# Performance work log

Hardware: AMD Instinct MI355X
Metric: run time of the kernel (lower is better)

Reference implementation:

```python
import jax, jax.numpy as jnp
import numpy as np

NUM_CLASSES = [5, 7, 4, 6, 3, 8, 5, 4, 6, 7, 3, 5, 4, 6, 8, 5, 7, 4, 6, 3]
N_ONE_HOTS = 20
N_OTHERS = 30
H = 48
W = 48
B = 128
N_MAP = 32
ENC_OUT = 32
RES_C = 128
OH_EMB = 9
SUM_NC = sum(NUM_CLASSES)  # 106


def conv2d(x, w, b=None, pad=0):
    # x: NCHW, w: OIHW
    y = jax.lax.conv_general_dilated(
        x, w, window_strides=(1, 1), padding=[(pad, pad), (pad, pad)],
        dimension_numbers=('NCHW', 'OIHW', 'NCHW'))
    if b is not None:
        y = y + b[None, :, None, None]
    return y


def setup_inputs() -> dict:
    key = jax.random.key(0)
    ks = jax.random.split(key, 20)
    x = jax.random.normal(ks[0], (B, 1 + N_MAP, H, W), dtype=jnp.float32)
    # first N_ONE_HOTS entries of flattened channel 0 are categorical indices
    idx_cols = [jax.random.randint(jax.random.fold_in(ks[1], j), (B,), 0, nc)
                for j, nc in enumerate(NUM_CLASSES)]
    idx = jnp.stack(idx_cols, axis=1).astype(jnp.float32)  # (B, 20)
    x = x.at[:, 0, 0, :N_ONE_HOTS].set(idx)
    s = 0.05
    inp = {
        'x': x,
        'fc_w': jax.random.normal(ks[2], (OH_EMB, SUM_NC), jnp.float32) * s,
        'fc_b': jnp.zeros((OH_EMB,), jnp.float32),
        'oh_conv_w': jax.random.normal(ks[3], (OH_EMB, OH_EMB, 1, 1), jnp.float32) * s,
        'oh_conv_b': jnp.zeros((OH_EMB,), jnp.float32),
        'others_conv_w': jax.random.normal(ks[4], (N_OTHERS, N_OTHERS, 1, 1), jnp.float32) * s,
        'others_conv_b': jnp.zeros((N_OTHERS,), jnp.float32),
        'all_conv_w': jax.random.normal(ks[5], (ENC_OUT, OH_EMB + N_OTHERS, 1, 1), jnp.float32) * s,
        'all_conv_b': jnp.zeros((ENC_OUT,), jnp.float32),
        'conv1_w': jax.random.normal(ks[6], (RES_C, ENC_OUT + N_MAP, 1, 1), jnp.float32) * s,
        'conv1_b': jnp.zeros((RES_C,), jnp.float32),
        'rconv1_w': jax.random.normal(ks[7], (RES_C, RES_C, 5, 5), jnp.float32) * s,
        'rconv1_b': jnp.zeros((RES_C,), jnp.float32),
        'rconv2_w': jax.random.normal(ks[8], (RES_C, RES_C, 5, 5), jnp.float32) * s,
        'rconv2_b': jnp.zeros((RES_C,), jnp.float32),
        'se_w1': jax.random.normal(ks[9], (RES_C // 16, RES_C), jnp.float32) * s,
        'se_w2': jax.random.normal(ks[10], (RES_C, RES_C // 16), jnp.float32) * s,
    }
    return inp


def reference(x, fc_w, fc_b, oh_conv_w, oh_conv_b, others_conv_w, others_conv_b,
              all_conv_w, all_conv_b, conv1_w, conv1_b, rconv1_w, rconv1_b,
              rconv2_w, rconv2_b, se_w1, se_w2):
    b = x.shape[0]
    gi = x[:, 0].reshape(b, -1)                 # (b, H*W)
    map_feature = x[:, 1:]                      # (b, N_MAP, H, W)
    idx = jax.lax.stop_gradient(gi[:, :N_ONE_HOTS]).astype(jnp.int32)
    others = gi[:, N_ONE_HOTS:N_ONE_HOTS + N_OTHERS]   # (b, 30)
    # vectorized one-hot build (replaces the quadratic python loop)
    oh = jnp.concatenate(
        [jax.nn.one_hot(idx[:, j], nc, dtype=x.dtype) for j, nc in enumerate(NUM_CLASSES)],
        axis=1)                                 # (b, SUM_NC)
    v = oh @ fc_w.T + fc_b                      # (b, 9)
    # faithful torch expand((h,w)+shape).reshape((b,-1,h,w)) semantics
    v = jnp.broadcast_to(v, (H, W, b, OH_EMB)).reshape(b, OH_EMB, H, W)
    o = jnp.broadcast_to(others, (H, W, b, N_OTHERS)).reshape(b, N_OTHERS, H, W)
    v = conv2d(v, oh_conv_w, oh_conv_b)
    o = conv2d(o, others_conv_w, others_conv_b)
    gi_map = conv2d(jnp.concatenate([v, o], axis=1), all_conv_w, all_conv_b)  # (b, 32, H, W)
    h = conv2d(jnp.concatenate([gi_map, map_feature], axis=1), conv1_w, conv1_b)  # (b, 128, H, W)
    # residual block: 5x5 convs, LeakyReLU, SE, identity skip (in==out)
    identity = h
    y = jax.nn.leaky_relu(conv2d(h, rconv1_w, rconv1_b, pad=2))
    y = conv2d(y, rconv2_w, rconv2_b, pad=2)
    s = y.mean(axis=(2, 3))                     # (b, 128)
    s = jax.nn.sigmoid(jax.nn.relu(s @ se_w1.T) @ se_w2.T)
    y = y * s[:, :, None, None]
    return jax.nn.leaky_relu(y + identity)
```

## Files before the change

### kernel.cpp

```cpp
#include <hip/hip_runtime.h>
#include <hip/hip_bf16.h>
#include <cstddef>

#define HH 48
#define WW 48
#define PIX 2304
#define BB 128
#define RESC 128
#define XCH 33

typedef short bf16x8 __attribute__((ext_vector_type(8)));
typedef float f32x4 __attribute__((ext_vector_type(4)));

static __device__ __forceinline__ float b2f(unsigned short u) {
    unsigned x = ((unsigned)u) << 16;
    return __builtin_bit_cast(float, x);
}
static __device__ __forceinline__ unsigned short f2b(float f) {
    __hip_bfloat16 hb = __float2bfloat16(f);
    return __builtin_bit_cast(unsigned short, hb);
}

__global__ void k_compute_v(const float* __restrict__ x, const float* __restrict__ fc_w,
                            const float* __restrict__ fc_b, float* __restrict__ v) {
    int b = blockIdx.x * blockDim.x + threadIdx.x;
    if (b >= BB) return;
    const int off[20] = {0,5,12,16,22,25,33,38,42,48,55,58,63,67,73,81,86,93,97,103};
    const float* gi = x + (size_t)b * XCH * PIX;
    int cols[20];
    #pragma unroll
    for (int j = 0; j < 20; j++) cols[j] = off[j] + (int)gi[j];
    #pragma unroll
    for (int e = 0; e < 9; e++) {
        float acc = fc_b[e];
        #pragma unroll
        for (int j = 0; j < 20; j++) acc += fc_w[e * 106 + cols[j]];
        v[b * 9 + e] = acc;
    }
}

__global__ void k_compute_G(const float* __restrict__ x, const float* __restrict__ v,
                            const float* __restrict__ ohw, const float* __restrict__ ohb,
                            const float* __restrict__ otw, const float* __restrict__ otb,
                            const float* __restrict__ aw,  const float* __restrict__ ab,
                            const float* __restrict__ c1w, const float* __restrict__ c1b,
                            float* __restrict__ G) {
    int p = blockIdx.x * blockDim.x + threadIdx.x;
    if (p >= PIX) return;
    float sv = v[((p / 9) & 127) * 9 + (p % 9)];
    float om[30];
    #pragma unroll
    for (int c2 = 0; c2 < 30; c2++) {
        int tmp = c2 * 24 + p;
        int c = tmp % 30;
        int bb = (c2 * 76 + tmp / 30) & 127;
        om[c2] = x[(size_t)bb * XCH * PIX + 20 + c];
    }
    float v9[9];
    #pragma unroll
    for (int e = 0; e < 9; e++) {
        float srow = 0.f;
        #pragma unroll
        for (int e2 = 0; e2 < 9; e2++) srow += ohw[e * 9 + e2];
        v9[e] = ohb[e] + srow * sv;
    }
    float o30[30];
    #pragma unroll
    for (int c = 0; c < 30; c++) {
        float a = otb[c];
        #pragma unroll
        for (int c2 = 0; c2 < 30; c2++) a += otw[c * 30 + c2] * om[c2];
        o30[c] = a;
    }
    float gi32[32];
    #pragma unroll
    for (int g = 0; g < 32; g++) {
        float a = ab[g];
        #pragma unroll
        for (int e = 0; e < 9; e++) a += aw[g * 39 + e] * v9[e];
        #pragma unroll
        for (int c = 0; c < 30; c++) a += aw[g * 39 + 9 + c] * o30[c];
        gi32[g] = a;
    }
    for (int oc = 0; oc < 128; oc++) {
        float a = c1b[oc];
        #pragma unroll
        for (int g = 0; g < 32; g++) a += c1w[oc * 64 + g] * gi32[g];
        G[p * 128 + oc] = a;
    }
}

__global__ void k_convert_w(const float* __restrict__ w1, const float* __restrict__ w2,
                            __hip_bfloat16* __restrict__ wb1, __hip_bfloat16* __restrict__ wb2) {
    int i = blockIdx.x * 256 + threadIdx.x;
    if (i >= 25 * 128 * 128) return;
    int tap = i / 16384, r = i % 16384;
    int oc = r >> 7, ic = r & 127;
    size_t src = (size_t)(oc * 128 + ic) * 25 + tap;
    wb1[i] = __float2bfloat16(w1[src]);
    wb2[i] = __float2bfloat16(w2[src]);
}

__global__ __launch_bounds__(256) void k_conv1(const float* __restrict__ x, const float* __restrict__ c1w,
                                               const float* __restrict__ G, __hip_bfloat16* __restrict__ h) {
    __shared__ float xm[32][64];
    __shared__ float w1[32][128];
    int b = blockIdx.y, p0 = blockIdx.x * 64;
    int t = threadIdx.x;
    for (int i = t; i < 4096; i += 256) { int m = i >> 7, oc = i & 127; w1[m][oc] = c1w[oc * 64 + 32 + m]; }
    for (int i = t; i < 2048; i += 256) {
        int m = i >> 6, pix = i & 63;
        xm[m][pix] = x[(size_t)b * XCH * PIX + (size_t)(1 + m) * PIX + p0 + pix];
    }
    __syncthreads();
    int pix = t & 63, ocg = t >> 6;
    float acc[32] = {};
    for (int m = 0; m < 32; m++) {
        float xv = xm[m][pix];
        const float4* wr = (const float4*)&w1[m][ocg * 32];
        #pragma unroll
        for (int k4 = 0; k4 < 8; k4++) {
            float4 wv = wr[k4];
            acc[k4 * 4 + 0] += wv.x * xv; acc[k4 * 4 + 1] += wv.y * xv;
            acc[k4 * 4 + 2] += wv.z * xv; acc[k4 * 4 + 3] += wv.w * xv;
        }
    }
    size_t hb = ((size_t)b * PIX + p0 + pix) * 128 + ocg * 32;
    const float* gp = &G[(size_t)(p0 + pix) * 128 + ocg * 32];
    #pragma unroll
    for (int q = 0; q < 4; q++) {
        unsigned short u[8];
        #pragma unroll
        for (int j = 0; j < 8; j++) u[j] = f2b(acc[q * 8 + j] + gp[q * 8 + j]);
        *(uint4*)(&h[hb + q * 8]) = *(uint4*)u;
    }
}

template<bool LEAKY, bool MEAN>
__global__ __launch_bounds__(256, 2) void k_conv5_mfma(
        const __hip_bfloat16* __restrict__ in,
        const __hip_bfloat16* __restrict__ w,
        const float* __restrict__ bias,
        __hip_bfloat16* __restrict__ out,
        float* __restrict__ mean) {
    __shared__ __align__(16) char lds[20 * 20 * 64 * 2];
    int b = blockIdx.z, tile = blockIdx.x;
    int ty0 = (tile / 3) * 16, tx0 = (tile % 3) * 16;
    int t = threadIdx.x;
    int wave = t >> 6, lane = t & 63;
    int wm = wave & 1, wn = wave >> 1;
    int l15 = lane & 15, lg = lane >> 4;

    f32x4 acc[4][8] = {};
    const size_t inb = (size_t)b * PIX * 128;

    for (int icb = 0; icb < 128; icb += 64) {
        if (icb) __syncthreads();
        for (int i = t; i < 3200; i += 256) {
            int s = i >> 3, c16 = i & 7;
            int ry = s / 20, rx = s % 20;
            int gy = ty0 - 2 + ry, gx = tx0 - 2 + rx;
            uint4 val = {0, 0, 0, 0};
            if ((unsigned)gy < 48u && (unsigned)gx < 48u)
                val = *(const uint4*)(in + inb + (size_t)(gy * 48 + gx) * 128 + icb + c16 * 8);
            int byte = ((s << 7) + (c16 << 4)) ^ ((s & 7) << 4);
            *(uint4*)(lds + byte) = val;
        }
        __syncthreads();
        for (int tap = 0; tap < 25; ++tap) {
            int dy = tap / 5, dx = tap % 5;
            const __hip_bfloat16* wt = w + (size_t)tap * 16384 + (size_t)(wm * 64 + l15) * 128 + icb + lg * 8;
            #pragma unroll
            for (int kk = 0; kk < 64; kk += 32) {
                bf16x8 A[4];
                #pragma unroll
                for (int m = 0; m < 4; m++) {
                    uint4 av = *(const uint4*)(wt + m * 16 * 128 + kk);
                    A[m] = __builtin_bit_cast(bf16x8, av);
                }
                #pragma unroll
                for (int n = 0; n < 8; n++) {
                    int s = (wn * 8 + n + dy) * 20 + (l15 + dx);
                    int byte = ((s << 7) + ((kk + lg * 8) << 1)) ^ ((s & 7) << 4);
                    bf16x8 B = *(const bf16x8*)(lds + byte);
                    #pragma unroll
                    for (int m = 0; m < 4; m++)
                        acc[m][n] = __builtin_amdgcn_mfma_f32_16x16x32_bf16(A[m], B, acc[m][n], 0, 0, 0);
                }
            }
        }
    }

    #pragma unroll
    for (int m = 0; m < 4; m++) {
        int ocm = wm * 64 + m * 16 + lg * 4;
        float b0 = bias[ocm], b1 = bias[ocm + 1], b2 = bias[ocm + 2], b3 = bias[ocm + 3];
        float ps0 = 0, ps1 = 0, ps2 = 0, ps3 = 0;
        #pragma unroll
        for (int n = 0; n < 8; n++) {
            float v0 = acc[m][n][0] + b0, v1 = acc[m][n][1] + b1;
            float v2 = acc[m][n][2] + b2, v3 = acc[m][n][3] + b3;
            ps0 += v0; ps1 += v1; ps2 += v2; ps3 += v3;
            if (LEAKY) {
                v0 = v0 > 0.f ? v0 : 0.01f * v0; v1 = v1 > 0.f ? v1 : 0.01f * v1;
                v2 = v2 > 0.f ? v2 : 0.01f * v2; v3 = v3 > 0.f ? v3 : 0.01f * v3;
            }
            int gp = (ty0 + wn * 8 + n) * 48 + tx0 + l15;
            uint2 pk;
            pk.x = (unsigned)f2b(v0) | ((unsigned)f2b(v1) << 16);
            pk.y = (unsigned)f2b(v2) | ((unsigned)f2b(v3) << 16);
            *(uint2*)(out + inb + (size_t)gp * 128 + ocm) = pk;
        }
        if (MEAN) {
            #pragma unroll
            for (int mask = 1; mask < 16; mask <<= 1) {
                ps0 += __shfl_xor(ps0, mask);
                ps1 += __shfl_xor(ps1, mask);
                ps2 += __shfl_xor(ps2, mask);
                ps3 += __shfl_xor(ps3, mask);
            }
            if (l15 == 0) {
                atomicAdd(&mean[b * 128 + ocm], ps0);
                atomicAdd(&mean[b * 128 + ocm + 1], ps1);
                atomicAdd(&mean[b * 128 + ocm + 2], ps2);
                atomicAdd(&mean[b * 128 + ocm + 3], ps3);
            }
        }
    }
}

__global__ void k_se(const float* __restrict__ mean, const float* __restrict__ w1,
                     const float* __restrict__ w2, float* __restrict__ s) {
    __shared__ float m[128];
    __shared__ float tt[8];
    int b = blockIdx.x, t = threadIdx.x;
    m[t] = mean[b * RESC + t] * (1.0f / 2304.0f);
    __syncthreads();
    if (t < 8) {
        float a = 0.f;
        for (int i = 0; i < 128; i++) a += w1[t * 128 + i] * m[i];
        tt[t] = a > 0.f ? a : 0.f;
    }
    __syncthreads();
    float a = 0.f;
    #pragma unroll
    for (int r = 0; r < 8; r++) a += w2[t * 8 + r] * tt[r];
    s[b * RESC + t] = 1.f / (1.f + expf(-a));
}

__global__ __launch_bounds__(256) void k_final(const __hip_bfloat16* __restrict__ y2,
                                               const __hip_bfloat16* __restrict__ h,
                                               const float* __restrict__ sg, float* __restrict__ out) {
    __shared__ float sl[128];
    __shared__ float tile[64 * 129];
    int b = blockIdx.y, p0 = blockIdx.x * 64, t = threadIdx.x;
    if (t < 128) sl[t] = sg[b * 128 + t];
    __syncthreads();
    const size_t base = ((size_t)b * PIX + p0) * 128;
    #pragma unroll
    for (int k = 0; k < 4; ++k) {
        int j = t + k * 256;
        int pix = j >> 4, c = j & 15;
        uint4 yv = *(const uint4*)(y2 + base + (size_t)pix * 128 + c * 8);
        uint4 hv = *(const uint4*)(h + base + (size_t)pix * 128 + c * 8);
        const unsigned short* yp = (const unsigned short*)&yv;
        const unsigned short* hp = (const unsigned short*)&hv;
        #pragma unroll
        for (int jj = 0; jj < 8; ++jj) {
            int oc = c * 8 + jj;
            tile[pix * 129 + oc] = b2f(yp[jj]) * sl[oc] + b2f(hp[jj]);
        }
    }
    __syncthreads();
    int oc = t >> 1, xh = (t & 1) * 32;
    float ov[32];
    #pragma unroll
    for (int i = 0; i < 32; ++i) {
        float v = tile[(xh + i) * 129 + oc];
        ov[i] = v > 0.f ? v : 0.01f * v;
    }
    float* op = out + ((size_t)b * 128 + oc) * PIX + p0 + xh;
    #pragma unroll
    for (int q = 0; q < 8; ++q) ((float4*)op)[q] = *(float4*)&ov[q * 4];
}

extern "C" void kernel_launch(void* const* d_in, const int* in_sizes, int n_in,
                              void* d_out, int out_size, void* d_ws, size_t ws_size,
                              hipStream_t stream) {
    const float* x      = (const float*)d_in[0];
    const float* fc_w   = (const float*)d_in[1];
    const float* fc_b   = (const float*)d_in[2];
    const float* ohw    = (const float*)d_in[3];
    const float* ohb    = (const float*)d_in[4];
    const float* otw    = (const float*)d_in[5];
    const float* otb    = (const float*)d_in[6];
    const float* aw     = (const float*)d_in[7];
    const float* ab     = (const float*)d_in[8];
    const float* c1w    = (const float*)d_in[9];
    const float* c1b    = (const float*)d_in[10];
    const float* r1w    = (const float*)d_in[11];
    const float* r1b    = (const float*)d_in[12];
    const float* r2w    = (const float*)d_in[13];
    const float* r2b    = (const float*)d_in[14];
    const float* se_w1  = (const float*)d_in[15];
    const float* se_w2  = (const float*)d_in[16];

    const size_t planeb = (size_t)BB * PIX * 128 * sizeof(__hip_bfloat16);
    char* ws = (char*)d_ws;
    __hip_bfloat16* h   = (__hip_bfloat16*)ws;  ws += planeb;
    __hip_bfloat16* y1  = (__hip_bfloat16*)ws;  ws += planeb;
    __hip_bfloat16* y2  = (__hip_bfloat16*)ws;  ws += planeb;
    float* G    = (float*)ws;                   ws += (size_t)PIX * 128 * sizeof(float);
    float* v    = (float*)ws;                   ws += (size_t)BB * 9 * sizeof(float);
    __hip_bfloat16* wb1 = (__hip_bfloat16*)ws;  ws += (size_t)25 * 128 * 128 * sizeof(__hip_bfloat16);
    __hip_bfloat16* wb2 = (__hip_bfloat16*)ws;  ws += (size_t)25 * 128 * 128 * sizeof(__hip_bfloat16);
    float* mean = (float*)ws;                   ws += (size_t)BB * RESC * sizeof(float);
    float* sgate= (float*)ws;                   ws += (size_t)BB * RESC * sizeof(float);

    k_compute_v<<<1, 128, 0, stream>>>(x, fc_w, fc_b, v);
    k_compute_G<<<9, 256, 0, stream>>>(x, v, ohw, ohb, otw, otb, aw, ab, c1w, c1b, G);
    k_convert_w<<<1600, 256, 0, stream>>>(r1w, r2w, wb1, wb2);
    k_conv1<<<dim3(36, 128), 256, 0, stream>>>(x, c1w, G, h);
    k_conv5_mfma<true, false><<<dim3(9, 1, 128), 256, 0, stream>>>(h, wb1, r1b, y1, nullptr);
    hipMemsetAsync(mean, 0, (size_t)BB * RESC * sizeof(float), stream);
    k_conv5_mfma<false, true><<<dim3(9, 1, 128), 256, 0, stream>>>(y1, wb2, r2b, y2, mean);
    k_se<<<128, 128, 0, stream>>>(mean, se_w1, se_w2, sgate);
    k_final<<<dim3(36, 128), 256, 0, stream>>>(y2, h, sgate, (float*)d_out);
}
```

Baseline: 834.4 us.

## Pad activations, double-buffer conv5 LDS via direct global-to-LDS loads

Stores h and y1 in a zero-bordered 52x52 padded layout so the 5x5 conv halo loads need no bounds checks. Each conv5 block now stages its input through global_load_lds into two 32-channel LDS buffers, so the next channel chunk loads while MFMAs run on the current one. Weight fragments for the next tap are prefetched into registers ahead of use, and s_setprio is raised around the MFMA bursts. In exchange it adds a border-zeroing kernel, slightly larger buffers and more complex swizzled address arithmetic.

```diff
diff --git a/kernel.cpp b/kernel.cpp
--- a/kernel.cpp
+++ b/kernel.cpp
@@ -5,6 +5,7 @@
 #define HH 48
 #define WW 48
 #define PIX 2304
+#define PPIX 2704
 #define BB 128
 #define RESC 128
 #define XCH 33
@@ -20,6 +21,10 @@
     __hip_bfloat16 hb = __float2bfloat16(f);
     return __builtin_bit_cast(unsigned short, hb);
 }
+
+#define GLOAD_LDS16(gp, lp) __builtin_amdgcn_global_load_lds( \
+    (const __attribute__((address_space(1))) void*)(gp), \
+    (__attribute__((address_space(3))) void*)(lp), 16, 0, 0)
 
 __global__ void k_compute_v(const float* __restrict__ x, const float* __restrict__ fc_w,
                             const float* __restrict__ fc_b, float* __restrict__ v) {
@@ -101,6 +106,20 @@
     wb2[i] = __float2bfloat16(w2[src]);
 }
 
+__global__ void k_zero_border(__hip_bfloat16* __restrict__ a, __hip_bfloat16* __restrict__ b2) {
+    int img = blockIdx.x, t = threadIdx.x;
+    for (int j = t; j < 6400; j += 256) {
+        int pb = j >> 4, c16 = j & 15;
+        int y, x2;
+        if (pb < 208) { int q = pb / 52; y = q < 2 ? q : q + 48; x2 = pb % 52; }
+        else { int r = pb - 208; y = 2 + (r >> 2); int c = r & 3; x2 = c < 2 ? c : c + 48; }
+        size_t off = ((size_t)img * PPIX + y * 52 + x2) * 128 + c16 * 8;
+        uint4 z = {0, 0, 0, 0};
+        *(uint4*)(a + off) = z;
+        *(uint4*)(b2 + off) = z;
+    }
+}
+
 __global__ __launch_bounds__(256) void k_conv1(const float* __restrict__ x, const float* __restrict__ c1w,
                                                const float* __restrict__ G, __hip_bfloat16* __restrict__ h) {
     __shared__ float xm[32][64];
@@ -125,8 +144,10 @@
             acc[k4 * 4 + 2] += wv.z * xv; acc[k4 * 4 + 3] += wv.w * xv;
         }
     }
-    size_t hb = ((size_t)b * PIX + p0 + pix) * 128 + ocg * 32;
-    const float* gp = &G[(size_t)(p0 + pix) * 128 + ocg * 32];
+    int p = p0 + pix;
+    int py = p / 48, px2 = p % 48;
+    size_t hb = ((size_t)b * PPIX + (py + 2) * 52 + px2 + 2) * 128 + ocg * 32;
+    const float* gp = &G[(size_t)p * 128 + ocg * 32];
     #pragma unroll
     for (int q = 0; q < 4; q++) {
         unsigned short u[8];
@@ -136,68 +157,112 @@
     }
 }
 
-template<bool LEAKY, bool MEAN>
+template<bool LEAKY, bool MEAN, bool PADOUT>
 __global__ __launch_bounds__(256, 2) void k_conv5_mfma(
         const __hip_bfloat16* __restrict__ in,
         const __hip_bfloat16* __restrict__ w,
         const float* __restrict__ bias,
         __hip_bfloat16* __restrict__ out,
         float* __restrict__ mean) {
-    __shared__ __align__(16) char lds[20 * 20 * 64 * 2];
+    __shared__ __align__(16) char lds[2][25600];
     int b = blockIdx.z, tile = blockIdx.x;
     int ty0 = (tile / 3) * 16, tx0 = (tile % 3) * 16;
-    int t = threadIdx.x;
-    int wave = t >> 6, lane = t & 63;
+    int t = threadIdx.x, lane = t & 63, wave = t >> 6;
     int wm = wave & 1, wn = wave >> 1;
     int l15 = lane & 15, lg = lane >> 4;
 
+    const size_t inb = (size_t)b * PPIX * 128;
+    const __hip_bfloat16* wbase = w + (size_t)(wm * 64 + l15) * 128 + lg * 8;
+
+    int sbase[8];
+    #pragma unroll
+    for (int n = 0; n < 8; ++n) sbase[n] = (wn * 8 + n) * 20 + l15;
+
     f32x4 acc[4][8] = {};
-    const size_t inb = (size_t)b * PIX * 128;
-
-    for (int icb = 0; icb < 128; icb += 64) {
-        if (icb) __syncthreads();
-        for (int i = t; i < 3200; i += 256) {
-            int s = i >> 3, c16 = i & 7;
+
+    auto stage = [&](int buf, int icb2) {
+        #pragma unroll
+        for (int k = 0; k < 6; ++k) {
+            int sg = k * 256 + t;
+            int u = sg >> 3, j = sg & 7;
+            int bb = j ^ (u & 7);
+            int s = (u << 1) | (bb >> 2);
+            int lg2 = bb & 3;
             int ry = s / 20, rx = s % 20;
-            int gy = ty0 - 2 + ry, gx = tx0 - 2 + rx;
-            uint4 val = {0, 0, 0, 0};
-            if ((unsigned)gy < 48u && (unsigned)gx < 48u)
-                val = *(const uint4*)(in + inb + (size_t)(gy * 48 + gx) * 128 + icb + c16 * 8);
-            int byte = ((s << 7) + (c16 << 4)) ^ ((s & 7) << 4);
-            *(uint4*)(lds + byte) = val;
-        }
-        __syncthreads();
-        for (int tap = 0; tap < 25; ++tap) {
-            int dy = tap / 5, dx = tap % 5;
-            const __hip_bfloat16* wt = w + (size_t)tap * 16384 + (size_t)(wm * 64 + l15) * 128 + icb + lg * 8;
-            #pragma unroll
-            for (int kk = 0; kk < 64; kk += 32) {
-                bf16x8 A[4];
-                #pragma unroll
-                for (int m = 0; m < 4; m++) {
-                    uint4 av = *(const uint4*)(wt + m * 16 * 128 + kk);
-                    A[m] = __builtin_bit_cast(bf16x8, av);
-                }
-                #pragma unroll
-                for (int n = 0; n < 8; n++) {
-                    int s = (wn * 8 + n + dy) * 20 + (l15 + dx);
-                    int byte = ((s << 7) + ((kk + lg * 8) << 1)) ^ ((s & 7) << 4);
-                    bf16x8 B = *(const bf16x8*)(lds + byte);
-                    #pragma unroll
-                    for (int m = 0; m < 4; m++)
-                        acc[m][n] = __builtin_amdgcn_mfma_f32_16x16x32_bf16(A[m], B, acc[m][n], 0, 0, 0);
-                }
-            }
-        }
-    }
-
-    #pragma unroll
-    for (int m = 0; m < 4; m++) {
+            const __hip_bfloat16* gp = in + inb + (size_t)((ty0 + ry) * 52 + tx0 + rx) * 128 + icb2 + lg2 * 8;
+            char* lp = &lds[buf][(k * 256 + (wave << 6)) * 16];
+            GLOAD_LDS16(gp, lp);
+        }
+        if (wave == 0) {
+            int sg = 1536 + lane;
+            int u = sg >> 3, j = sg & 7;
+            int bb = j ^ (u & 7);
+            int s = (u << 1) | (bb >> 2);
+            int lg2 = bb & 3;
+            int ry = s / 20, rx = s % 20;
+            const __hip_bfloat16* gp = in + inb + (size_t)((ty0 + ry) * 52 + tx0 + rx) * 128 + icb2 + lg2 * 8;
+            char* lp = &lds[buf][1536 * 16];
+            GLOAD_LDS16(gp, lp);
+        }
+    };
+
+#define AISSUE(Areg, tap_) do { \
+        const __hip_bfloat16* wp = wbase + (size_t)(tap_) * 16384 + icb; \
+        Areg[0] = *(const bf16x8*)(wp); \
+        Areg[1] = *(const bf16x8*)(wp + 2048); \
+        Areg[2] = *(const bf16x8*)(wp + 4096); \
+        Areg[3] = *(const bf16x8*)(wp + 6144); \
+    } while (0)
+
+#define CTAP(Areg, tap_) do { \
+        int toff = (tap_) + 15 * ((tap_) / 5); \
+        __builtin_amdgcn_s_setprio(1); \
+        _Pragma("unroll") \
+        for (int n = 0; n < 8; ++n) { \
+            int s = sbase[n] + toff; \
+            int u = s >> 1; \
+            int jj = (((s & 1) << 2) | lg) ^ (u & 7); \
+            bf16x8 Bv = *(const bf16x8*)(cb + (u << 7) + (jj << 4)); \
+            acc[0][n] = __builtin_amdgcn_mfma_f32_16x16x32_bf16(Areg[0], Bv, acc[0][n], 0, 0, 0); \
+            acc[1][n] = __builtin_amdgcn_mfma_f32_16x16x32_bf16(Areg[1], Bv, acc[1][n], 0, 0, 0); \
+            acc[2][n] = __builtin_amdgcn_mfma_f32_16x16x32_bf16(Areg[2], Bv, acc[2][n], 0, 0, 0); \
+            acc[3][n] = __builtin_amdgcn_mfma_f32_16x16x32_bf16(Areg[3], Bv, acc[3][n], 0, 0, 0); \
+        } \
+        __builtin_amdgcn_s_setprio(0); \
+    } while (0)
+
+    stage(0, 0);
+    __syncthreads();
+
+    for (int c = 0; c < 4; ++c) {
+        const int icb = c * 32;
+        const char* cb = lds[c & 1];
+        bf16x8 A0[4], A1[4];
+        AISSUE(A0, 0);
+        AISSUE(A1, 1);
+        __builtin_amdgcn_sched_barrier(0);
+        if (c < 3) stage((c + 1) & 1, icb + 32);
+        __builtin_amdgcn_sched_barrier(0);
+        for (int i = 0; i < 12; ++i) {
+            int tp = 2 * i;
+            CTAP(A0, tp);
+            AISSUE(A0, tp + 2);
+            CTAP(A1, tp + 1);
+            AISSUE(A1, tp + 3);
+        }
+        CTAP(A0, 24);
+        if (c < 3) __syncthreads();
+    }
+#undef AISSUE
+#undef CTAP
+
+    #pragma unroll
+    for (int m = 0; m < 4; ++m) {
         int ocm = wm * 64 + m * 16 + lg * 4;
         float b0 = bias[ocm], b1 = bias[ocm + 1], b2 = bias[ocm + 2], b3 = bias[ocm + 3];
         float ps0 = 0, ps1 = 0, ps2 = 0, ps3 = 0;
         #pragma unroll
-        for (int n = 0; n < 8; n++) {
+        for (int n = 0; n < 8; ++n) {
             float v0 = acc[m][n][0] + b0, v1 = acc[m][n][1] + b1;
             float v2 = acc[m][n][2] + b2, v3 = acc[m][n][3] + b3;
             ps0 += v0; ps1 += v1; ps2 += v2; ps3 += v3;
@@ -205,11 +270,14 @@
                 v0 = v0 > 0.f ? v0 : 0.01f * v0; v1 = v1 > 0.f ? v1 : 0.01f * v1;
                 v2 = v2 > 0.f ? v2 : 0.01f * v2; v3 = v3 > 0.f ? v3 : 0.01f * v3;
             }
-            int gp = (ty0 + wn * 8 + n) * 48 + tx0 + l15;
+            int row = ty0 + wn * 8 + n, col = tx0 + l15;
+            size_t off;
+            if (PADOUT) off = ((size_t)b * PPIX + (row + 2) * 52 + col + 2) * 128 + ocm;
+            else        off = ((size_t)b * PIX + row * 48 + col) * 128 + ocm;
             uint2 pk;
             pk.x = (unsigned)f2b(v0) | ((unsigned)f2b(v1) << 16);
             pk.y = (unsigned)f2b(v2) | ((unsigned)f2b(v3) << 16);
-            *(uint2*)(out + inb + (size_t)gp * 128 + ocm) = pk;
+            *(uint2*)(out + off) = pk;
         }
         if (MEAN) {
             #pragma unroll
@@ -256,13 +324,14 @@
     int b = blockIdx.y, p0 = blockIdx.x * 64, t = threadIdx.x;
     if (t < 128) sl[t] = sg[b * 128 + t];
     __syncthreads();
-    const size_t base = ((size_t)b * PIX + p0) * 128;
     #pragma unroll
     for (int k = 0; k < 4; ++k) {
         int j = t + k * 256;
         int pix = j >> 4, c = j & 15;
-        uint4 yv = *(const uint4*)(y2 + base + (size_t)pix * 128 + c * 8);
-        uint4 hv = *(const uint4*)(h + base + (size_t)pix * 128 + c * 8);
+        int p = p0 + pix;
+        int py = p / 48, px2 = p % 48;
+        uint4 yv = *(const uint4*)(y2 + ((size_t)b * PIX + p) * 128 + c * 8);
+        uint4 hv = *(const uint4*)(h + ((size_t)b * PPIX + (py + 2) * 52 + px2 + 2) * 128 + c * 8);
         const unsigned short* yp = (const unsigned short*)&yv;
         const unsigned short* hp = (const unsigned short*)&hv;
         #pragma unroll
@@ -305,25 +374,27 @@
     const float* se_w1  = (const float*)d_in[15];
     const float* se_w2  = (const float*)d_in[16];
 
-    const size_t planeb = (size_t)BB * PIX * 128 * sizeof(__hip_bfloat16);
+    const size_t padb = (size_t)BB * PPIX * 128 * sizeof(__hip_bfloat16);
     char* ws = (char*)d_ws;
-    __hip_bfloat16* h   = (__hip_bfloat16*)ws;  ws += planeb;
-    __hip_bfloat16* y1  = (__hip_bfloat16*)ws;  ws += planeb;
-    __hip_bfloat16* y2  = (__hip_bfloat16*)ws;  ws += planeb;
-    float* G    = (float*)ws;                   ws += (size_t)PIX * 128 * sizeof(float);
-    float* v    = (float*)ws;                   ws += (size_t)BB * 9 * sizeof(float);
-    __hip_bfloat16* wb1 = (__hip_bfloat16*)ws;  ws += (size_t)25 * 128 * 128 * sizeof(__hip_bfloat16);
-    __hip_bfloat16* wb2 = (__hip_bfloat16*)ws;  ws += (size_t)25 * 128 * 128 * sizeof(__hip_bfloat16);
-    float* mean = (float*)ws;                   ws += (size_t)BB * RESC * sizeof(float);
-    float* sgate= (float*)ws;                   ws += (size_t)BB * RESC * sizeof(float);
+    __hip_bfloat16* h    = (__hip_bfloat16*)ws;  ws += padb;
+    __hip_bfloat16* y1   = (__hip_bfloat16*)ws;  ws += padb;
+    __hip_bfloat16* y2   = (__hip_bfloat16*)ws;  ws += (size_t)BB * PIX * 128 * sizeof(__hip_bfloat16);
+    float* G    = (float*)ws;                    ws += (size_t)PIX * 128 * sizeof(float);
+    float* v    = (float*)ws;                    ws += (size_t)BB * 9 * sizeof(float);
+    __hip_bfloat16* wb1 = (__hip_bfloat16*)ws;   ws += (size_t)25 * 128 * 128 * sizeof(__hip_bfloat16);
+    __hip_bfloat16* wb2 = (__hip_bfloat16*)ws;   ws += (size_t)25 * 128 * 128 * sizeof(__hip_bfloat16);
+    ws += 131072;
+    float* mean = (float*)ws;                    ws += (size_t)BB * RESC * sizeof(float);
+    float* sgate= (float*)ws;                    ws += (size_t)BB * RESC * sizeof(float);
 
     k_compute_v<<<1, 128, 0, stream>>>(x, fc_w, fc_b, v);
     k_compute_G<<<9, 256, 0, stream>>>(x, v, ohw, ohb, otw, otb, aw, ab, c1w, c1b, G);
     k_convert_w<<<1600, 256, 0, stream>>>(r1w, r2w, wb1, wb2);
+    k_zero_border<<<128, 256, 0, stream>>>(h, y1);
     k_conv1<<<dim3(36, 128), 256, 0, stream>>>(x, c1w, G, h);
-    k_conv5_mfma<true, false><<<dim3(9, 1, 128), 256, 0, stream>>>(h, wb1, r1b, y1, nullptr);
+    k_conv5_mfma<true, false, true><<<dim3(9, 1, 128), 256, 0, stream>>>(h, wb1, r1b, y1, nullptr);
     hipMemsetAsync(mean, 0, (size_t)BB * RESC * sizeof(float), stream);
-    k_conv5_mfma<false, true><<<dim3(9, 1, 128), 256, 0, stream>>>(y1, wb2, r2b, y2, mean);
+    k_conv5_mfma<false, true, false><<<dim3(9, 1, 128), 256, 0, stream>>>(y1, wb2, r2b, y2, mean);
     k_se<<<128, 128, 0, stream>>>(mean, se_w1, se_w2, sgate);
     k_final<<<dim3(36, 128), 256, 0, stream>>>(y2, h, sgate, (float*)d_out);
 }
```

Result: faster. 812.8 us (-2.6%).
